# Performance work log

Hardware: AMD Instinct MI355X
Metric: run time of the kernel (lower is better)

The kernel has to match this reference:

```python
import jax, jax.numpy as jnp
import numpy as np
from jax import lax

HEADS = 8

def rotate_every_two(x):
    x1 = x[..., ::2]
    x2 = x[..., 1::2]
    return jnp.stack([-x2, x1], axis=-1).reshape(x.shape)

def theta_shift(x, sin, cos):
    # x: (b,n,N,d); sin/cos: (N,d) broadcast over b,n
    return x * cos + rotate_every_two(x) * sin

def setup_inputs() -> dict:
    key = jax.random.key(0)
    ks = jax.random.split(key, 8)
    B, C, H, W = 8, 256, 64, 64
    hd = C // HEADS
    return {
        'x': jax.random.normal(ks[0], (B, C, H, W), jnp.float32),
        'sin': jax.random.normal(ks[1], (H * W, hd), jnp.float32),
        'cos': jax.random.normal(ks[2], (H * W, hd), jnp.float32),
        'w_qkvo': jax.random.normal(ks[3], (4 * C, C), jnp.float32) * 0.02,
        'b_qkvo': jnp.zeros((4 * C,), jnp.float32),
        'w_lepe': jax.random.normal(ks[4], (C, 1, 5, 5), jnp.float32) * 0.02,
        'b_lepe': jnp.zeros((C,), jnp.float32),
        'w_proj': jax.random.normal(ks[5], (C, C), jnp.float32) * 0.02,
        'b_proj': jnp.zeros((C,), jnp.float32),
    }

def reference(x, sin, cos, w_qkvo, b_qkvo, w_lepe, b_lepe, w_proj, b_proj):
    B, C, H, W = x.shape
    heads = HEADS
    hd = C // heads
    N = H * W
    scale = hd ** (-0.5)

    # 1x1 conv qkvo
    qkvo = jnp.einsum('bchw,oc->bohw', x, w_qkvo) + b_qkvo[None, :, None, None]
    qkv = qkvo[:, :3 * C]
    o = qkvo[:, 3 * C:]

    # depthwise 5x5 lepe on v channels
    v_img = qkv[:, 2 * C:]
    lepe = lax.conv_general_dilated(
        v_img, w_lepe, (1, 1), [(2, 2), (2, 2)],
        dimension_numbers=('NCHW', 'OIHW', 'NCHW'),
        feature_group_count=C) + b_lepe[None, :, None, None]

    # b (m n d) h w -> m b n (h w) d
    qkv_r = qkv.reshape(B, 3, heads, hd, N).transpose(1, 0, 2, 4, 3)
    q, k, v = qkv_r[0], qkv_r[1], qkv_r[2]  # (b,n,N,d)

    q = jax.nn.elu(q) + 1.0
    k = jax.nn.elu(k) + 1.0

    # z = q @ mean_k^T * scale -> (b,n,N,1)
    z = jnp.einsum('bnld,bnd->bnl', q, k.mean(axis=2))[..., None] * scale

    q = theta_shift(q, sin, cos)
    k = theta_shift(k, sin, cos)

    s = (scale / N) ** 0.5
    kv = jnp.einsum('bnld,bnle->bnde', k * s, v * s)  # (b,n,d,d)
    v_mean = v.mean(axis=2, keepdims=True)  # (b,n,1,d)

    res = jnp.einsum('bnld,bnde->bnle', q, kv) * (1.0 + 1.0 / (z + 1e-6)) - z * v_mean

    # b n (h w) d -> b (n d) h w
    res = res.transpose(0, 1, 3, 2).reshape(B, C, H, W)
    res = res + lepe

    out = jnp.einsum('bchw,oc->bohw', res * o, w_proj) + b_proj[None, :, None, None]
    return out
```

## Files before the change

kernel.cpp:

```cpp
#include <hip/hip_runtime.h>
#include <hip/hip_bf16.h>

typedef unsigned short u16;
typedef unsigned int u32;
typedef short bf16x8 __attribute__((ext_vector_type(8)));
typedef float f32x4 __attribute__((ext_vector_type(4)));
typedef u32 u32x4 __attribute__((ext_vector_type(4)));

#define N_TOK 4096
#define C_DIM 256
#define HEADS 8
#define HD 32
#define SCALE_F 0.17677669529663687f

__device__ inline u16 f2bf(float f) {
    u32 u = __float_as_uint(f);
    u += 0x7fffu + ((u >> 16) & 1u);
    return (u16)(u >> 16);
}
__device__ inline float b2f(u16 h) { return __uint_as_float((u32)h << 16); }
__device__ inline float bf_lo(u32 u) { return __uint_as_float(u << 16); }
__device__ inline float bf_hi(u32 u) { return __uint_as_float(u & 0xffff0000u); }

__device__ inline void gload16(const void* g, void* l) {
    __builtin_amdgcn_global_load_lds((const __attribute__((address_space(1))) u32*)g,
                                     (__attribute__((address_space(3))) u32*)l, 16, 0, 0);
}

__device__ inline void store_out(float* p, float v) { *p = v; }
__device__ inline void store_out(u16* p, float v) { *p = f2bf(v); }

__global__ __launch_bounds__(256) void stage1(const float* __restrict__ x, const float* __restrict__ w1,
                                              const float* __restrict__ w2, const float* __restrict__ s,
                                              const float* __restrict__ c, u16* __restrict__ xT,
                                              u16* __restrict__ o1, u16* __restrict__ o2, u32* __restrict__ scT) {
    __shared__ char smem[16896];
    int bx = blockIdx.x;
    int t = threadIdx.x;
    if (bx < 8192) {
        int lt = bx & 127, ct = (bx >> 7) & 7, b = bx >> 10;
        int c0 = ct * 32, l0 = lt * 32;
        const float* xb = x + ((size_t)b * C_DIM + c0) * N_TOK + l0;
        u16 (*tl)[33] = (u16(*)[33])smem;
        int li = t & 31, ci = t >> 5;
#pragma unroll
        for (int i = 0; i < 4; ++i)
            tl[ci + i * 8][li] = f2bf(xb[(size_t)(ci + i * 8) * N_TOK + li]);
        __syncthreads();
        int c2 = t & 15, lr = t >> 4;
        u16* outp = xT + ((size_t)b * N_TOK + l0) * C_DIM + c0;
#pragma unroll
        for (int i = 0; i < 2; ++i) {
            int l = lr + i * 16;
            u32 pv = (u32)tl[2 * c2][l] | ((u32)tl[2 * c2 + 1][l] << 16);
            *(u32*)(outp + (size_t)l * C_DIM + 2 * c2) = pv;
        }
        return;
    }
    int px = bx - 8192;
    if (px < 1024) {
        int i = px * 256 + t;
        o1[i] = f2bf(w1[i]);
        if (i < 256 * 256) o2[i] = f2bf(w2[i]);
        return;
    }
    int l0 = (px - 1024) * 64;
    float (*ts)[33] = (float(*)[33])smem;
    float (*tc)[33] = (float(*)[33])(smem + 8448);
    int d = t & 31, r = t >> 5;
#pragma unroll
    for (int i = 0; i < 8; ++i) {
        ts[r + i * 8][d] = s[(size_t)(l0 + r + i * 8) * HD + d];
        tc[r + i * 8][d] = c[(size_t)(l0 + r + i * 8) * HD + d];
    }
    __syncthreads();
    int li = t & 63, dr = t >> 6;
#pragma unroll
    for (int i = 0; i < 8; ++i) {
        int dd = dr * 8 + i;
        scT[(size_t)dd * N_TOK + l0 + li] = (u32)f2bf(ts[li][dd]) | ((u32)f2bf(tc[li][dd]) << 16);
    }
}

template <typename TO>
__global__ __launch_bounds__(256) void gemm_bt(const u16* __restrict__ A, const u16* __restrict__ Bm,
                                               const float* __restrict__ bias, TO* __restrict__ C,
                                               int M, int L, int K) {
    int bt = blockIdx.z;
    int m0 = blockIdx.y * 128;
    int l0 = blockIdx.x * 128;
    const u16* Bb = Bm + (size_t)bt * L * K;
    TO* Cb = C + (size_t)bt * M * L;

    __shared__ u16 smem[17408];
    u16* As = smem;
    u16* Bs = smem + 8192;
    u16* Cs = smem;

    int t = threadIdx.x;
    int w = t >> 6, lane = t & 63;
    int wr = (w >> 1) * 64, wc = (w & 1) * 64;
    int fr = lane & 15, kg = lane >> 4;

    f32x4 acc[4][4] = {};

    for (int k0 = 0; k0 < K; k0 += 64) {
#pragma unroll
        for (int j = 0; j < 4; ++j) {
            int c = j * 256 + w * 64 + lane;
            int row = c >> 3, slot = c & 7;
            int gslot = slot ^ (row & 7);
            u16* abase = As + (size_t)(j * 256 + w * 64) * 8;
            u16* bbase = Bs + (size_t)(j * 256 + w * 64) * 8;
            gload16(A + (size_t)(m0 + row) * K + k0 + gslot * 8, abase);
            gload16(Bb + (size_t)(l0 + row) * K + k0 + gslot * 8, bbase);
        }
        __syncthreads();
#pragma unroll
        for (int kk = 0; kk < 2; ++kk) {
            bf16x8 af[4], bfr[4];
#pragma unroll
            for (int i = 0; i < 4; ++i) {
                int ra = wr + i * 16 + fr;
                int rb = wc + i * 16 + fr;
                af[i]  = *(const bf16x8*)(As + (size_t)ra * 64 + (size_t)((kk * 4 + kg) ^ (ra & 7)) * 8);
                bfr[i] = *(const bf16x8*)(Bs + (size_t)rb * 64 + (size_t)((kk * 4 + kg) ^ (rb & 7)) * 8);
            }
#pragma unroll
            for (int i = 0; i < 4; ++i)
#pragma unroll
                for (int jj = 0; jj < 4; ++jj)
                    acc[i][jj] = __builtin_amdgcn_mfma_f32_16x16x32_bf16(af[i], bfr[jj], acc[i][jj], 0, 0, 0);
        }
        __syncthreads();
    }

    int rg = (lane >> 4) * 4;
    if constexpr (sizeof(TO) == 2) {
#pragma unroll
        for (int i = 0; i < 4; ++i)
#pragma unroll
            for (int jj = 0; jj < 4; ++jj) {
                int col = wc + jj * 16 + fr;
#pragma unroll
                for (int r = 0; r < 4; ++r) {
                    int row = wr + i * 16 + rg + r;
                    Cs[row * 136 + col] = f2bf(acc[i][jj][r] + bias[m0 + row]);
                }
            }
        __syncthreads();
        u16* CbT = (u16*)Cb;
#pragma unroll
        for (int j = 0; j < 8; ++j) {
            int id = j * 256 + t;
            int row = id >> 4, c8 = (id & 15) * 8;
            *(uint4*)(CbT + (size_t)(m0 + row) * L + l0 + c8) = *(const uint4*)(Cs + row * 136 + c8);
        }
    } else {
#pragma unroll
        for (int i = 0; i < 4; ++i)
#pragma unroll
            for (int jj = 0; jj < 4; ++jj) {
                int col = l0 + wc + jj * 16 + fr;
#pragma unroll
                for (int r = 0; r < 4; ++r) {
                    int row = m0 + wr + i * 16 + rg + r;
                    store_out(Cb + (size_t)row * L + col, acc[i][jj][r] + bias[row]);
                }
            }
    }
}

__global__ __launch_bounds__(256) void stage2(const u16* __restrict__ qkvo, const u32* __restrict__ scT,
                                              const float* __restrict__ wl, const float* __restrict__ bl,
                                              float* __restrict__ part_kv, float* __restrict__ part_ks,
                                              float* __restrict__ part_vs, u16* __restrict__ lepe) {
    __shared__ char smem[34048];
    int bx = blockIdx.x;
    int t = threadIdx.x;

    if (bx >= 1024) {
        int i2 = bx - 1024;
        int c = i2 & 255, b = i2 >> 8;
        const u16* src = qkvo + ((size_t)b * 1024 + 512 + c) * N_TOK;
        u16* dst = lepe + ((size_t)b * C_DIM + c) * N_TOK;
        float* wc5 = (float*)smem;
        if (t < 25) wc5[t] = wl[c * 25 + t];
        __syncthreads();

        int h = t >> 2, w0 = (t & 3) * 16;
        float bb = bl[c];
        float o16[16];
#pragma unroll
        for (int i = 0; i < 16; ++i) o16[i] = bb;

#pragma unroll
        for (int dh = 0; dh < 5; ++dh) {
            int gr = h + dh - 2;
            bool rowok = (gr >= 0) && (gr < 64);
            const u16* rp = src + (size_t)(rowok ? gr : 0) * 64 + w0 - 8;
            bf16x8 L0 = ((const bf16x8*)rp)[0];
            bf16x8 L1 = ((const bf16x8*)rp)[1];
            bf16x8 L2 = ((const bf16x8*)rp)[2];
            bf16x8 L3 = ((const bf16x8*)rp)[3];
            float rbuf[32];
#pragma unroll
            for (int j = 0; j < 32; ++j) {
                int col = w0 - 8 + j;
                u16 raw = (u16)(j < 8 ? L0[j] : j < 16 ? L1[j - 8] : j < 24 ? L2[j - 16] : L3[j - 24]);
                bool ok = rowok && (col >= 0) && (col < 64);
                rbuf[j] = ok ? b2f(raw) : 0.f;
            }
#pragma unroll
            for (int dw = 0; dw < 5; ++dw) {
                float wv_ = wc5[dh * 5 + dw];
#pragma unroll
                for (int ow = 0; ow < 16; ++ow)
                    o16[ow] += rbuf[6 + dw + ow] * wv_;
            }
        }

        uint4 u0, u1;
        u0.x = (u32)f2bf(o16[0]) | ((u32)f2bf(o16[1]) << 16);
        u0.y = (u32)f2bf(o16[2]) | ((u32)f2bf(o16[3]) << 16);
        u0.z = (u32)f2bf(o16[4]) | ((u32)f2bf(o16[5]) << 16);
        u0.w = (u32)f2bf(o16[6]) | ((u32)f2bf(o16[7]) << 16);
        u1.x = (u32)f2bf(o16[8]) | ((u32)f2bf(o16[9]) << 16);
        u1.y = (u32)f2bf(o16[10]) | ((u32)f2bf(o16[11]) << 16);
        u1.z = (u32)f2bf(o16[12]) | ((u32)f2bf(o16[13]) << 16);
        u1.w = (u32)f2bf(o16[14]) | ((u32)f2bf(o16[15]) << 16);
        *(uint4*)(dst + h * 64 + w0) = u0;
        *(uint4*)(dst + h * 64 + w0 + 8) = u1;
        return;
    }

    int chunk = bx & 15, bn = bx >> 4;
    int b = bn >> 3, n = bn & 7;
    const u16* kp = qkvo + ((size_t)b * 1024 + 256 + n * HD) * N_TOK;
    const u16* vp = qkvo + ((size_t)b * 1024 + 512 + n * HD) * N_TOK;
    int lbase = chunk * 256;

    u16 (*ks_bf)[136] = (u16(*)[136])smem;
    u16 (*v_bf)[136]  = (u16(*)[136])(smem + 8704);
    float* red  = (float*)(smem + 17408);
    float* redk = (float*)(smem + 33792);
    float* redv = (float*)(smem + 33920);

    int w = t >> 6, lane = t & 63;
    int fr = lane & 15, kg = lane >> 4;
    int p = t >> 4, g = t & 15;
    int dv = t >> 3, g2 = t & 7;

    f32x4 acc[2][2] = {};
    float ks0 = 0.f, ks1 = 0.f, vs = 0.f;

    for (int st = 0; st < 2; ++st) {
        int tok0 = lbase + st * 128;
        if (st) __syncthreads();
        const u16* k0p = kp + (size_t)(2 * p) * N_TOK + tok0 + g * 8;
        const u16* k1p = k0p + N_TOK;
        const u32* s0p = scT + (size_t)(2 * p) * N_TOK + tok0 + g * 8;
        const u32* s1p = s0p + N_TOK;
        bf16x8 k0 = *(const bf16x8*)k0p;
        bf16x8 k1 = *(const bf16x8*)k1p;
        u32x4 s0a = ((const u32x4*)s0p)[0], s0b = ((const u32x4*)s0p)[1];
        u32x4 s1a = ((const u32x4*)s1p)[0], s1b = ((const u32x4*)s1p)[1];
        const u16* vpp = vp + (size_t)dv * N_TOK + tok0 + g2 * 16;
        bf16x8 va = ((const bf16x8*)vpp)[0];
        bf16x8 vb = ((const bf16x8*)vpp)[1];

        u16 o0[8], o1[8];
#pragma unroll
        for (int j = 0; j < 8; ++j) {
            float kv0 = b2f((u16)k0[j]);
            float kv1 = b2f((u16)k1[j]);
            u32 sc0 = j < 4 ? s0a[j] : s0b[j - 4];
            u32 sc1 = j < 4 ? s1a[j] : s1b[j - 4];
            float e0 = kv0 > 0.f ? kv0 + 1.f : __expf(kv0);
            float e1 = kv1 > 0.f ? kv1 + 1.f : __expf(kv1);
            ks0 += e0; ks1 += e1;
            float se = bf_lo(sc0), ce = bf_hi(sc0);
            float so = bf_lo(sc1), co = bf_hi(sc1);
            o0[j] = f2bf(e0 * ce - e1 * se);
            o1[j] = f2bf(e1 * co + e0 * so);
        }
        u32x4 w0, w1;
#pragma unroll
        for (int q = 0; q < 4; ++q) {
            w0[q] = (u32)o0[2 * q] | ((u32)o0[2 * q + 1] << 16);
            w1[q] = (u32)o1[2 * q] | ((u32)o1[2 * q + 1] << 16);
        }
        *(u32x4*)&ks_bf[2 * p][g * 8] = w0;
        *(u32x4*)&ks_bf[2 * p + 1][g * 8] = w1;

#pragma unroll
        for (int j = 0; j < 8; ++j) { vs += b2f((u16)va[j]); }
#pragma unroll
        for (int j = 0; j < 8; ++j) { vs += b2f((u16)vb[j]); }
        *(bf16x8*)&v_bf[dv][g2 * 16] = va;
        *(bf16x8*)&v_bf[dv][g2 * 16 + 8] = vb;
        __syncthreads();

        int kcol = w * 32 + kg * 8;
        bf16x8 af[2], bfv[2];
#pragma unroll
        for (int i = 0; i < 2; ++i) {
            af[i]  = *(const bf16x8*)&ks_bf[i * 16 + fr][kcol];
            bfv[i] = *(const bf16x8*)&v_bf[i * 16 + fr][kcol];
        }
#pragma unroll
        for (int i = 0; i < 2; ++i)
#pragma unroll
            for (int jj = 0; jj < 2; ++jj)
                acc[i][jj] = __builtin_amdgcn_mfma_f32_16x16x32_bf16(af[i], bfv[jj], acc[i][jj], 0, 0, 0);
    }

#pragma unroll
    for (int i = 0; i < 2; ++i)
#pragma unroll
        for (int jj = 0; jj < 2; ++jj)
#pragma unroll
            for (int r = 0; r < 4; ++r) {
                int row = i * 16 + kg * 4 + r;
                int col = jj * 16 + fr;
                red[w * 1024 + row * 32 + col] = acc[i][jj][r];
            }

#pragma unroll
    for (int m = 1; m < 16; m <<= 1) {
        ks0 += __shfl_xor(ks0, m);
        ks1 += __shfl_xor(ks1, m);
    }
    if ((lane & 15) == 0) { redk[2 * p] = ks0; redk[2 * p + 1] = ks1; }
#pragma unroll
    for (int m = 1; m < 8; m <<= 1) vs += __shfl_xor(vs, m);
    if ((lane & 7) == 0) redv[dv] = vs;
    __syncthreads();

    float* pkv = part_kv + ((size_t)bn * 16 + chunk) * 1024;
#pragma unroll
    for (int i = 0; i < 4; ++i) {
        int el = i * 256 + t;
        pkv[el] = red[el] + red[1024 + el] + red[2048 + el] + red[3072 + el];
    }
    if (t < 32) {
        part_ks[((size_t)bn * 16 + chunk) * 32 + t] = redk[t];
        part_vs[((size_t)bn * 16 + chunk) * 32 + t] = redv[t];
    }
}

__global__ __launch_bounds__(256) void kv_final(const float* __restrict__ part_kv, const float* __restrict__ part_ks,
                                                const float* __restrict__ part_vs, u16* __restrict__ kvT_bf,
                                                float* __restrict__ kmean, float* __restrict__ vmean) {
    int bn = blockIdx.x;
    int t = threadIdx.x;
    const float* p = part_kv + (size_t)bn * 16 * 1024;
    const float s2c = SCALE_F / (float)N_TOK;
#pragma unroll
    for (int i = 0; i < 4; ++i) {
        int sl = t + i * 256;
        float s = 0;
#pragma unroll
        for (int c = 0; c < 16; ++c) s += p[(size_t)c * 1024 + sl];
        float val = s * s2c;
        int d = sl >> 5, e = sl & 31;
        kvT_bf[(size_t)bn * 1024 + e * 32 + d] = f2bf(val);
    }
    if (t < 32) {
        float s = 0, sv = 0;
        for (int c = 0; c < 16; ++c) {
            s  += part_ks[((size_t)bn * 16 + c) * 32 + t];
            sv += part_vs[((size_t)bn * 16 + c) * 32 + t];
        }
        kmean[bn * 32 + t] = s * (1.f / (float)N_TOK);
        vmean[bn * 32 + t] = sv * (1.f / (float)N_TOK);
    }
}

__global__ __launch_bounds__(256) void attn_epilogue(const u16* __restrict__ qkvo, const u32* __restrict__ scT,
                                                     const u16* __restrict__ kvT_bf, const float* __restrict__ kmean,
                                                     const float* __restrict__ vmean, const u16* __restrict__ lepe,
                                                     u16* __restrict__ resnT) {
    int lt = blockIdx.x, bn = blockIdx.y;
    int b = bn >> 3, n = bn & 7;
    const u16* qp = qkvo + ((size_t)b * 1024 + n * HD) * N_TOK;
    const u16* op = qkvo + ((size_t)b * 1024 + 768 + n * HD) * N_TOK;
    const u16* lp = lepe + ((size_t)b * C_DIM + n * HD) * N_TOK;

    __shared__ u16 kvb[32 * 40];
    __shared__ float kml[32], vml[32];
    __shared__ u16 Atile[4][64 * 40];
    __shared__ float Rtile[4][64 * 36];

    int t = threadIdx.x;
    int w = t >> 6, lane = t & 63;

    if (t < 128) {
        int e = t >> 2, d0 = (t & 3) * 8;
        *(uint4*)(kvb + e * 40 + d0) = *(const uint4*)(kvT_bf + (size_t)bn * 1024 + e * 32 + d0);
    }
    if (t < 32) { kml[t] = kmean[bn * 32 + t]; vml[t] = vmean[bn * 32 + t]; }
    __syncthreads();

    int token = lt * 256 + w * 64 + lane;

    float qv[32];
    float z = 0.f;
#pragma unroll
    for (int d = 0; d < 32; ++d) {
        float x_ = b2f(qp[(size_t)d * N_TOK + token]);
        float e_ = x_ > 0.f ? x_ + 1.f : __expf(x_);
        qv[d] = e_;
        z += e_ * kml[d];
    }
    z *= SCALE_F;
#pragma unroll
    for (int p = 0; p < 16; ++p) {
        u32 sc0 = scT[(size_t)(2 * p) * N_TOK + token];
        u32 sc1 = scT[(size_t)(2 * p + 1) * N_TOK + token];
        float se = bf_lo(sc0), ce = bf_hi(sc0);
        float so = bf_lo(sc1), co = bf_hi(sc1);
        float a = qv[2 * p], bb = qv[2 * p + 1];
        qv[2 * p]     = a * ce - bb * se;
        qv[2 * p + 1] = bb * co + a * so;
    }
    float mult = 1.f + 1.f / (z + 1e-6f);

    u16* Aw = Atile[w];
#pragma unroll
    for (int j4 = 0; j4 < 4; ++j4) {
        uint4 u;
        u.x = (u32)f2bf(qv[8 * j4 + 0]) | ((u32)f2bf(qv[8 * j4 + 1]) << 16);
        u.y = (u32)f2bf(qv[8 * j4 + 2]) | ((u32)f2bf(qv[8 * j4 + 3]) << 16);
        u.z = (u32)f2bf(qv[8 * j4 + 4]) | ((u32)f2bf(qv[8 * j4 + 5]) << 16);
        u.w = (u32)f2bf(qv[8 * j4 + 6]) | ((u32)f2bf(qv[8 * j4 + 7]) << 16);
        *(uint4*)(Aw + lane * 40 + j4 * 8) = u;
    }
    __syncthreads();

    int fr = lane & 15, kg = lane >> 4;
    bf16x8 af[4], bfr[2];
#pragma unroll
    for (int i = 0; i < 4; ++i)
        af[i] = *(const bf16x8*)(Aw + (i * 16 + fr) * 40 + kg * 8);
#pragma unroll
    for (int jj = 0; jj < 2; ++jj)
        bfr[jj] = *(const bf16x8*)(kvb + (jj * 16 + fr) * 40 + kg * 8);

    float* Rw = Rtile[w];
    f32x4 zero = {0.f, 0.f, 0.f, 0.f};
#pragma unroll
    for (int i = 0; i < 4; ++i)
#pragma unroll
        for (int jj = 0; jj < 2; ++jj) {
            f32x4 acc = __builtin_amdgcn_mfma_f32_16x16x32_bf16(af[i], bfr[jj], zero, 0, 0, 0);
#pragma unroll
            for (int r = 0; r < 4; ++r)
                Rw[(i * 16 + kg * 4 + r) * 36 + jj * 16 + fr] = acc[r];
        }
    __syncthreads();

    float res[32];
#pragma unroll
    for (int j = 0; j < 8; ++j) {
        f32x4 vr = *(const f32x4*)(Rw + lane * 36 + j * 4);
        res[4 * j] = vr[0]; res[4 * j + 1] = vr[1]; res[4 * j + 2] = vr[2]; res[4 * j + 3] = vr[3];
    }

    u16* dst0 = resnT + ((size_t)b * N_TOK + token) * C_DIM + n * HD;
#pragma unroll
    for (int g = 0; g < 4; ++g) {
        float vv[8];
#pragma unroll
        for (int e2 = 0; e2 < 8; ++e2) {
            int ee = g * 8 + e2;
            float lx = b2f(lp[(size_t)ee * N_TOK + token]);
            float ov = b2f(op[(size_t)ee * N_TOK + token]);
            float rx = res[ee] * mult - z * vml[ee];
            vv[e2] = (rx + lx) * ov;
        }
        uint4 u;
        u.x = (u32)f2bf(vv[0]) | ((u32)f2bf(vv[1]) << 16);
        u.y = (u32)f2bf(vv[2]) | ((u32)f2bf(vv[3]) << 16);
        u.z = (u32)f2bf(vv[4]) | ((u32)f2bf(vv[5]) << 16);
        u.w = (u32)f2bf(vv[6]) | ((u32)f2bf(vv[7]) << 16);
        ((uint4*)(dst0 + g * 8))[0] = u;
    }
}

extern "C" void kernel_launch(void* const* d_in, const int* in_sizes, int n_in,
                              void* d_out, int out_size, void* d_ws, size_t ws_size,
                              hipStream_t stream) {
    const float* x      = (const float*)d_in[0];
    const float* sinp   = (const float*)d_in[1];
    const float* cosp   = (const float*)d_in[2];
    const float* w_qkvo = (const float*)d_in[3];
    const float* b_qkvo = (const float*)d_in[4];
    const float* w_lepe = (const float*)d_in[5];
    const float* b_lepe = (const float*)d_in[6];
    const float* w_proj = (const float*)d_in[7];
    const float* b_proj = (const float*)d_in[8];

    char* ws = (char*)d_ws;
    size_t off = 0;
    auto alloc = [&](size_t bytes) { size_t o = off; off = (off + bytes + 255) & ~(size_t)255; return o; };
    u16*   wbf     = (u16*)(ws + alloc((size_t)1024 * 256 * 2));
    u16*   wpbf    = (u16*)(ws + alloc((size_t)256 * 256 * 2));
    u16*   xT      = (u16*)(ws + alloc((size_t)8 * 4096 * 256 * 2));
    u16*   qkvo    = (u16*)(ws + alloc((size_t)8 * 1024 * 4096 * 2));
    u16*   lepe    = (u16*)(ws + alloc((size_t)8 * 256 * 4096 * 2));
    u16*   resnT   = (u16*)(ws + alloc((size_t)8 * 4096 * 256 * 2));
    float* part_kv = (float*)(ws + alloc((size_t)64 * 16 * 1024 * 4));
    float* part_ks = (float*)(ws + alloc((size_t)64 * 16 * 32 * 4));
    float* part_vs = (float*)(ws + alloc((size_t)64 * 16 * 32 * 4));
    u16*   kvT_bf  = (u16*)(ws + alloc((size_t)64 * 1024 * 2));
    float* kmean   = (float*)(ws + alloc((size_t)64 * 32 * 4));
    float* vmean   = (float*)(ws + alloc((size_t)64 * 32 * 4));
    u32*   scT     = (u32*)(ws + alloc((size_t)32 * 4096 * 4));
    if (off > ws_size) return;

    stage1<<<dim3(9280), dim3(256), 0, stream>>>(x, w_qkvo, w_proj, sinp, cosp, xT, wbf, wpbf, scT);
    gemm_bt<u16><<<dim3(32, 8, 8), dim3(256), 0, stream>>>(wbf, xT, b_qkvo, qkvo, 1024, 4096, 256);
    stage2<<<dim3(3072), dim3(256), 0, stream>>>(qkvo, scT, w_lepe, b_lepe, part_kv, part_ks, part_vs, lepe);
    kv_final<<<dim3(64), dim3(256), 0, stream>>>(part_kv, part_ks, part_vs, kvT_bf, kmean, vmean);
    attn_epilogue<<<dim3(16, 64), dim3(256), 0, stream>>>(qkvo, scT, kvT_bf, kmean, vmean, lepe, resnT);
    gemm_bt<float><<<dim3(32, 2, 8), dim3(256), 0, stream>>>(wpbf, resnT, b_proj, (float*)d_out, 256, 4096, 256);
}
```

Baseline: 101.6 us.

## Fuse q and o projections into attention epilogue, shrink qkvo GEMM to k,v

The first GEMM now computes only the k and v channels (512 rows) into a smaller buffer. The q and o projections for each head are recomputed inside the attention epilogue with an MFMA GEMM over x tiles staged in LDS. This removes the global write and re-read of q and o activations (half of the qkvo tensor). In exchange the epilogue gains GEMM work, larger LDS use (about 64KB, which lowers occupancy), and rounds the kv result tile to bf16.

```diff
diff --git a/kernel.cpp b/kernel.cpp
--- a/kernel.cpp
+++ b/kernel.cpp
@@ -171,7 +171,7 @@
     }
 }
 
-__global__ __launch_bounds__(256) void stage2(const u16* __restrict__ qkvo, const u32* __restrict__ scT,
+__global__ __launch_bounds__(256) void stage2(const u16* __restrict__ qkv, const u32* __restrict__ scT,
                                               const float* __restrict__ wl, const float* __restrict__ bl,
                                               float* __restrict__ part_kv, float* __restrict__ part_ks,
                                               float* __restrict__ part_vs, u16* __restrict__ lepe) {
@@ -182,7 +182,7 @@
     if (bx >= 1024) {
         int i2 = bx - 1024;
         int c = i2 & 255, b = i2 >> 8;
-        const u16* src = qkvo + ((size_t)b * 1024 + 512 + c) * N_TOK;
+        const u16* src = qkv + ((size_t)b * 512 + 256 + c) * N_TOK;
         u16* dst = lepe + ((size_t)b * C_DIM + c) * N_TOK;
         float* wc5 = (float*)smem;
         if (t < 25) wc5[t] = wl[c * 25 + t];
@@ -236,8 +236,8 @@
 
     int chunk = bx & 15, bn = bx >> 4;
     int b = bn >> 3, n = bn & 7;
-    const u16* kp = qkvo + ((size_t)b * 1024 + 256 + n * HD) * N_TOK;
-    const u16* vp = qkvo + ((size_t)b * 1024 + 512 + n * HD) * N_TOK;
+    const u16* kp = qkv + ((size_t)b * 512 + n * HD) * N_TOK;
+    const u16* vp = qkv + ((size_t)b * 512 + 256 + n * HD) * N_TOK;
     int lbase = chunk * 256;
 
     u16 (*ks_bf)[136] = (u16(*)[136])smem;
@@ -377,41 +377,106 @@
     }
 }
 
-__global__ __launch_bounds__(256) void attn_epilogue(const u16* __restrict__ qkvo, const u32* __restrict__ scT,
+__global__ __launch_bounds__(256) void attn_epilogue(const u16* __restrict__ wbf, const float* __restrict__ bq,
+                                                     const u16* __restrict__ xT, const u32* __restrict__ scT,
                                                      const u16* __restrict__ kvT_bf, const float* __restrict__ kmean,
                                                      const float* __restrict__ vmean, const u16* __restrict__ lepe,
                                                      u16* __restrict__ resnT) {
     int lt = blockIdx.x, bn = blockIdx.y;
     int b = bn >> 3, n = bn & 7;
-    const u16* qp = qkvo + ((size_t)b * 1024 + n * HD) * N_TOK;
-    const u16* op = qkvo + ((size_t)b * 1024 + 768 + n * HD) * N_TOK;
+    int T0 = lt * 256;
     const u16* lp = lepe + ((size_t)b * C_DIM + n * HD) * N_TOK;
-
-    __shared__ u16 kvb[32 * 40];
-    __shared__ float kml[32], vml[32];
-    __shared__ u16 Atile[4][64 * 40];
-    __shared__ float Rtile[4][64 * 36];
+    const u16* Bx = xT + ((size_t)b * N_TOK + T0) * C_DIM;
+
+    __shared__ char smem[64256];
+    u16* qA    = (u16*)smem;
+    u16* o_lds = (u16*)(smem + 20480);
+    u16* Rt    = (u16*)(smem + 40960);
+    u16* kvb   = (u16*)(smem + 61440);
+    float* kml = (float*)(smem + 64000);
+    float* vml = (float*)(smem + 64128);
+    u16* Bst = (u16*)smem;
+    u16* Ast = (u16*)(smem + 32768);
 
     int t = threadIdx.x;
     int w = t >> 6, lane = t & 63;
+    int fr = lane & 15, kg = lane >> 4;
 
     if (t < 128) {
         int e = t >> 2, d0 = (t & 3) * 8;
         *(uint4*)(kvb + e * 40 + d0) = *(const uint4*)(kvT_bf + (size_t)bn * 1024 + e * 32 + d0);
     }
     if (t < 32) { kml[t] = kmean[bn * 32 + t]; vml[t] = vmean[bn * 32 + t]; }
+
+    f32x4 acc[4][4] = {};
+    for (int k0 = 0; k0 < 256; k0 += 64) {
+#pragma unroll
+        for (int j = 0; j < 8; ++j) {
+            int c = j * 256 + w * 64 + lane;
+            int row = c >> 3, slot = c & 7;
+            int gslot = slot ^ (row & 7);
+            gload16(Bx + (size_t)row * C_DIM + k0 + gslot * 8, Bst + (size_t)(j * 256 + w * 64) * 8);
+        }
+#pragma unroll
+        for (int j = 0; j < 2; ++j) {
+            int c = j * 256 + w * 64 + lane;
+            int row = c >> 3, slot = c & 7;
+            int gslot = slot ^ (row & 7);
+            int arow = (row < 32 ? n * HD : 736 + n * HD) + row;
+            gload16(wbf + (size_t)arow * C_DIM + k0 + gslot * 8, Ast + (size_t)(j * 256 + w * 64) * 8);
+        }
+        __syncthreads();
+#pragma unroll
+        for (int kk = 0; kk < 2; ++kk) {
+            bf16x8 af[4], bfr[4];
+#pragma unroll
+            for (int i = 0; i < 4; ++i) {
+                int ra = i * 16 + fr;
+                af[i] = *(const bf16x8*)(Ast + (size_t)ra * 64 + (size_t)((kk * 4 + kg) ^ (ra & 7)) * 8);
+            }
+#pragma unroll
+            for (int jj = 0; jj < 4; ++jj) {
+                int rb = w * 64 + jj * 16 + fr;
+                bfr[jj] = *(const bf16x8*)(Bst + (size_t)rb * 64 + (size_t)((kk * 4 + kg) ^ (rb & 7)) * 8);
+            }
+#pragma unroll
+            for (int i = 0; i < 4; ++i)
+#pragma unroll
+                for (int jj = 0; jj < 4; ++jj)
+                    acc[i][jj] = __builtin_amdgcn_mfma_f32_16x16x32_bf16(af[i], bfr[jj], acc[i][jj], 0, 0, 0);
+        }
+        __syncthreads();
+    }
+    int rg = kg * 4;
+#pragma unroll
+    for (int i = 0; i < 4; ++i)
+#pragma unroll
+        for (int jj = 0; jj < 4; ++jj) {
+            int tok = w * 64 + jj * 16 + fr;
+#pragma unroll
+            for (int r = 0; r < 4; ++r) {
+                int qorow = i * 16 + rg + r;
+                int brow = (qorow < 32 ? n * HD : 736 + n * HD) + qorow;
+                u16 val = f2bf(acc[i][jj][r] + bq[brow]);
+                if (qorow < 32) qA[tok * 40 + qorow] = val;
+                else            o_lds[tok * 40 + qorow - 32] = val;
+            }
+        }
     __syncthreads();
 
-    int token = lt * 256 + w * 64 + lane;
-
+    int token = T0 + t;
     float qv[32];
     float z = 0.f;
 #pragma unroll
-    for (int d = 0; d < 32; ++d) {
-        float x_ = b2f(qp[(size_t)d * N_TOK + token]);
-        float e_ = x_ > 0.f ? x_ + 1.f : __expf(x_);
-        qv[d] = e_;
-        z += e_ * kml[d];
+    for (int j = 0; j < 4; ++j) {
+        bf16x8 q8 = *(const bf16x8*)(qA + t * 40 + j * 8);
+#pragma unroll
+        for (int e = 0; e < 8; ++e) {
+            float x_ = b2f((u16)q8[e]);
+            float e_ = x_ > 0.f ? x_ + 1.f : __expf(x_);
+            qv[j * 8 + e] = e_;
+            z += e_ * kml[j * 8 + e];
+        }
     }
     z *= SCALE_F;
 #pragma unroll
@@ -425,8 +490,6 @@
         qv[2 * p + 1] = bb * co + a * so;
     }
     float mult = 1.f + 1.f / (z + 1e-6f);
-
-    u16* Aw = Atile[w];
 #pragma unroll
     for (int j4 = 0; j4 < 4; ++j4) {
         uint4 u;
@@ -434,37 +497,43 @@
         u.y = (u32)f2bf(qv[8 * j4 + 2]) | ((u32)f2bf(qv[8 * j4 + 3]) << 16);
         u.z = (u32)f2bf(qv[8 * j4 + 4]) | ((u32)f2bf(qv[8 * j4 + 5]) << 16);
         u.w = (u32)f2bf(qv[8 * j4 + 6]) | ((u32)f2bf(qv[8 * j4 + 7]) << 16);
-        *(uint4*)(Aw + lane * 40 + j4 * 8) = u;
+        *(uint4*)(qA + t * 40 + j4 * 8) = u;
     }
     __syncthreads();
 
-    int fr = lane & 15, kg = lane >> 4;
-    bf16x8 af[4], bfr[2];
-#pragma unroll
-    for (int i = 0; i < 4; ++i)
-        af[i] = *(const bf16x8*)(Aw + (i * 16 + fr) * 40 + kg * 8);
-#pragma unroll
-    for (int jj = 0; jj < 2; ++jj)
-        bfr[jj] = *(const bf16x8*)(kvb + (jj * 16 + fr) * 40 + kg * 8);
-
-    float* Rw = Rtile[w];
-    f32x4 zero = {0.f, 0.f, 0.f, 0.f};
-#pragma unroll
-    for (int i = 0; i < 4; ++i)
-#pragma unroll
-        for (int jj = 0; jj < 2; ++jj) {
-            f32x4 acc = __builtin_amdgcn_mfma_f32_16x16x32_bf16(af[i], bfr[jj], zero, 0, 0, 0);
-#pragma unroll
-            for (int r = 0; r < 4; ++r)
-                Rw[(i * 16 + kg * 4 + r) * 36 + jj * 16 + fr] = acc[r];
-        }
+    {
+        bf16x8 af[4], bfr[2];
+#pragma unroll
+        for (int i = 0; i < 4; ++i)
+            af[i] = *(const bf16x8*)(qA + (size_t)(w * 64 + i * 16 + fr) * 40 + kg * 8);
+#pragma unroll
+        for (int jj = 0; jj < 2; ++jj)
+            bfr[jj] = *(const bf16x8*)(kvb + (jj * 16 + fr) * 40 + kg * 8);
+
+        u16* Rw = Rt + w * 2560;
+        f32x4 zero = {0.f, 0.f, 0.f, 0.f};
+#pragma unroll
+        for (int i = 0; i < 4; ++i)
+#pragma unroll
+            for (int jj = 0; jj < 2; ++jj) {
+                f32x4 a2 = __builtin_amdgcn_mfma_f32_16x16x32_bf16(af[i], bfr[jj], zero, 0, 0, 0);
+#pragma unroll
+                for (int r = 0; r < 4; ++r)
+                    Rw[(i * 16 + kg * 4 + r) * 40 + jj * 16 + fr] = f2bf(a2[r]);
+            }
+    }
     __syncthreads();
 
-    float res[32];
-#pragma unroll
-    for (int j = 0; j < 8; ++j) {
-        f32x4 vr = *(const f32x4*)(Rw + lane * 36 + j * 4);
-        res[4 * j] = vr[0]; res[4 * j + 1] = vr[1]; res[4 * j + 2] = vr[2]; res[4 * j + 3] = vr[3];
+    float res[32], ovv[32];
+#pragma unroll
+    for (int j = 0; j < 4; ++j) {
+        bf16x8 r8 = *(const bf16x8*)(Rt + w * 2560 + lane * 40 + j * 8);
+        bf16x8 o8 = *(const bf16x8*)(o_lds + t * 40 + j * 8);
+#pragma unroll
+        for (int e = 0; e < 8; ++e) {
+            res[j * 8 + e] = b2f((u16)r8[e]);
+            ovv[j * 8 + e] = b2f((u16)o8[e]);
+        }
     }
 
     u16* dst0 = resnT + ((size_t)b * N_TOK + token) * C_DIM + n * HD;
@@ -475,9 +544,8 @@
         for (int e2 = 0; e2 < 8; ++e2) {
             int ee = g * 8 + e2;
             float lx = b2f(lp[(size_t)ee * N_TOK + token]);
-            float ov = b2f(op[(size_t)ee * N_TOK + token]);
             float rx = res[ee] * mult - z * vml[ee];
-            vv[e2] = (rx + lx) * ov;
+            vv[e2] = (rx + lx) * ovv[ee];
         }
         uint4 u;
         u.x = (u32)f2bf(vv[0]) | ((u32)f2bf(vv[1]) << 16);
@@ -507,7 +575,7 @@
     u16*   wbf     = (u16*)(ws + alloc((size_t)1024 * 256 * 2));
     u16*   wpbf    = (u16*)(ws + alloc((size_t)256 * 256 * 2));
     u16*   xT      = (u16*)(ws + alloc((size_t)8 * 4096 * 256 * 2));
-    u16*   qkvo    = (u16*)(ws + alloc((size_t)8 * 1024 * 4096 * 2));
+    u16*   qkv     = (u16*)(ws + alloc((size_t)8 * 512 * 4096 * 2));
     u16*   lepe    = (u16*)(ws + alloc((size_t)8 * 256 * 4096 * 2));
     u16*   resnT   = (u16*)(ws + alloc((size_t)8 * 4096 * 256 * 2));
     float* part_kv = (float*)(ws + alloc((size_t)64 * 16 * 1024 * 4));
@@ -520,9 +588,9 @@
     if (off > ws_size) return;
 
     stage1<<<dim3(9280), dim3(256), 0, stream>>>(x, w_qkvo, w_proj, sinp, cosp, xT, wbf, wpbf, scT);
-    gemm_bt<u16><<<dim3(32, 8, 8), dim3(256), 0, stream>>>(wbf, xT, b_qkvo, qkvo, 1024, 4096, 256);
-    stage2<<<dim3(3072), dim3(256), 0, stream>>>(qkvo, scT, w_lepe, b_lepe, part_kv, part_ks, part_vs, lepe);
+    gemm_bt<u16><<<dim3(32, 4, 8), dim3(256), 0, stream>>>(wbf + 256 * 256, xT, b_qkvo + 256, qkv, 512, 4096, 256);
+    stage2<<<dim3(3072), dim3(256), 0, stream>>>(qkv, scT, w_lepe, b_lepe, part_kv, part_ks, part_vs, lepe);
     kv_final<<<dim3(64), dim3(256), 0, stream>>>(part_kv, part_ks, part_vs, kvT_bf, kmean, vmean);
-    attn_epilogue<<<dim3(16, 64), dim3(256), 0, stream>>>(qkvo, scT, kvT_bf, kmean, vmean, lepe, resnT);
+    attn_epilogue<<<dim3(16, 64), dim3(256), 0, stream>>>(wbf, b_qkvo, xT, scT, kvT_bf, kmean, vmean, lepe, resnT);
     gemm_bt<float><<<dim3(32, 2, 8), dim3(256), 0, stream>>>(wpbf, resnT, b_proj, (float*)d_out, 256, 4096, 256);
 }
```

Result: faster. 95.04 us (-6.4%).
